# Kernel optimization log

Hardware: AMD Instinct MI355X
Metric: run time of the kernel (lower is better)

Reference implementation:

```python
import jax, jax.numpy as jnp
import numpy as np

D_MODEL = 1024
N_HEADS = 16
D_HEAD = D_MODEL // N_HEADS
B, S = 2, 2048


def setup_inputs() -> dict:
    key = jax.random.key(0)
    ks = jax.random.split(key, 8)
    scale = 1.0 / np.sqrt(D_MODEL)
    return {
        "x": jax.random.normal(ks[0], (B, S, D_MODEL), dtype=jnp.float32),
        "Wq": jax.random.normal(ks[1], (D_MODEL, D_MODEL), dtype=jnp.float32) * scale,
        "bq": jnp.zeros((D_MODEL,), dtype=jnp.float32),
        "Wk": jax.random.normal(ks[2], (D_MODEL, D_MODEL), dtype=jnp.float32) * scale,
        "bk": jnp.zeros((D_MODEL,), dtype=jnp.float32),
        "Wv": jax.random.normal(ks[3], (D_MODEL, D_MODEL), dtype=jnp.float32) * scale,
        "bv": jnp.zeros((D_MODEL,), dtype=jnp.float32),
        "Wo": jax.random.normal(ks[4], (D_MODEL, D_MODEL), dtype=jnp.float32) * scale,
    }


def reference(x, Wq, bq, Wk, bk, Wv, bv, Wo):
    Bsz, Slen, D = x.shape
    # projections -> [B, H, S, Dh]
    def split_heads(t):
        return t.reshape(Bsz, Slen, N_HEADS, D_HEAD).transpose(0, 2, 1, 3)
    q = split_heads(x @ Wq + bq)
    k = split_heads(x @ Wk + bk)
    v = split_heads(x @ Wv + bv)
    scale = jnp.sqrt(jnp.float32(D_HEAD))
    scores = jnp.einsum('bhsd,bhtd->bhst', q, k) / scale  # [B,H,S,S]
    causal_mask = jnp.tril(jnp.ones((Slen, Slen), dtype=jnp.bool_))
    scores = jnp.where(causal_mask, scores, jnp.finfo(scores.dtype).min)
    attn = jax.nn.softmax(scores, axis=-1)
    # deterministic=True path: dropout is identity
    out = jnp.einsum('bhst,bhtd->bhsd', attn, v)
    out = out.transpose(0, 2, 1, 3).reshape(Bsz, Slen, D)
    return out @ Wo
```

## Files before the change

### kernel.cpp

```cpp
#include <hip/hip_runtime.h>
#include <hip/hip_bf16.h>

#define BATCH   2
#define SEQ     2048
#define DMODEL  1024
#define NHEADS  16
#define DHEAD   64
#define MROWS   (BATCH*SEQ)
#define NBH     (BATCH*NHEADS)

typedef float  f32x4  __attribute__((ext_vector_type(4)));
typedef short  s16x4  __attribute__((ext_vector_type(4)));
typedef short  s16x8  __attribute__((ext_vector_type(8)));
typedef __bf16 bf16x8 __attribute__((ext_vector_type(8)));

__device__ __forceinline__ short f2bf(float f) {
  union { float f; unsigned u; } v; v.f = f;
  return (short)((v.u + 0x7fffu + ((v.u >> 16) & 1u)) >> 16);
}
__device__ __forceinline__ float bf2f(short s) {
  union { unsigned u; float f; } v; v.u = ((unsigned)(unsigned short)s) << 16;
  return v.f;
}

__global__ void prep_fused(const float* __restrict__ x, short* __restrict__ xb,
                           const float* __restrict__ Wq, const float* __restrict__ Wk,
                           const float* __restrict__ Wv, const float* __restrict__ Wo,
                           short* __restrict__ WtQKV, short* __restrict__ WtO) {
  __shared__ float t[32][33];
  int z = blockIdx.z;
  int tx = threadIdx.x, ty = threadIdx.y;
  if (z >= 4) {
    int blk = (z - 4) * 1024 + blockIdx.y * 32 + blockIdx.x;
    int i = (blk * 256 + ty * 32 + tx) * 4;
    float4 v = *(const float4*)(x + i);
    s16x4 o = { f2bf(v.x), f2bf(v.y), f2bf(v.z), f2bf(v.w) };
    *(s16x4*)(xb + i) = o;
    return;
  }
  const float* W; short* Wt;
  if      (z == 0) { W = Wq; Wt = WtQKV; }
  else if (z == 1) { W = Wk; Wt = WtQKV + (1u << 20); }
  else if (z == 2) { W = Wv; Wt = WtQKV + (2u << 20); }
  else             { W = Wo; Wt = WtO; }
  int n0 = blockIdx.x * 32, k0 = blockIdx.y * 32;
  #pragma unroll
  for (int i = 0; i < 32; i += 8) t[ty + i][tx] = W[(k0 + ty + i) * DMODEL + n0 + tx];
  __syncthreads();
  #pragma unroll
  for (int i = 0; i < 32; i += 8) Wt[(n0 + ty + i) * DMODEL + k0 + tx] = f2bf(t[tx][ty + i]);
}

template<int MT, int NT, int EPI>
__global__ __launch_bounds__(256) void gemm_bf16(
    const short* __restrict__ A, const short* __restrict__ Bt,
    const float* __restrict__ bq, const float* __restrict__ bk, const float* __restrict__ bv,
    short* __restrict__ qb, short* __restrict__ kb, short* __restrict__ vt,
    float* __restrict__ out)
{
  constexpr int K = DMODEL, BK = 32;
  constexpr int WM = MT / 2, WN = NT / 2;
  constexpr int TM = WM / 16, TN = WN / 16;
  constexpr int CA = MT * BK / 512;
  constexpr int CB = NT * BK / 512;
  constexpr int TP = 136;
  constexpr int SME = (EPI == 0) ? 128 * TP : (MT * BK + NT * BK);
  __shared__ short smem[SME];
  short* la = smem;
  short* lb = smem + MT * BK;
  const int tid = threadIdx.x;
  const int wave = tid >> 6, lane = tid & 63;
  const int quad = lane >> 4, l16 = lane & 15;
  const int wr = wave >> 1, wc = wave & 1;
  const int nx = gridDim.x, ny = gridDim.y;
  const int g = blockIdx.y * nx + blockIdx.x;
  const int xcd = g & 7, rr = g >> 3;
  const int m0 = (xcd * (ny >> 3) + rr / nx) * MT;
  const int n0 = (rr % nx) * NT;
  const int arow = lane >> 2, acol = (lane & 3) * 8;

  f32x4 acc[TM][TN] = {};

  for (int k0 = 0; k0 < K; k0 += BK) {
    for (int c = wave; c < CA; c += 4) {
      const short* gp = A + (m0 + c * 16 + arow) * K + k0 + acol;
      __builtin_amdgcn_global_load_lds((__attribute__((address_space(1))) void*)gp,
                                       (__attribute__((address_space(3))) void*)(la + c * 512),
                                       16, 0, 0);
    }
    for (int c = wave; c < CB; c += 4) {
      const short* gp = Bt + (n0 + c * 16 + arow) * K + k0 + acol;
      __builtin_amdgcn_global_load_lds((__attribute__((address_space(1))) void*)gp,
                                       (__attribute__((address_space(3))) void*)(lb + c * 512),
                                       16, 0, 0);
    }
    __syncthreads();
    bf16x8 af[TM], bfr[TN];
    #pragma unroll
    for (int i = 0; i < TM; ++i)
      af[i] = *(const bf16x8*)&la[(wr * WM + i * 16 + l16) * BK + quad * 8];
    #pragma unroll
    for (int j = 0; j < TN; ++j)
      bfr[j] = *(const bf16x8*)&lb[(wc * WN + j * 16 + l16) * BK + quad * 8];
    #pragma unroll
    for (int i = 0; i < TM; ++i)
      #pragma unroll
      for (int j = 0; j < TN; ++j)
        acc[i][j] = __builtin_amdgcn_mfma_f32_16x16x32_bf16(af[i], bfr[j], acc[i][j], 0, 0, 0);
    __syncthreads();
  }

  if constexpr (EPI == 0) {
    const bool isV = (n0 >= 2 * DMODEL);
    const float* bias; int nbase; float scl;
    if (n0 < DMODEL)          { bias = bq; nbase = 0;          scl = 0.125f * 1.44269504089f; }
    else if (n0 < 2 * DMODEL) { bias = bk; nbase = DMODEL;     scl = 1.f; }
    else                      { bias = bv; nbase = 2 * DMODEL; scl = 1.f; }
    #pragma unroll
    for (int j = 0; j < TN; ++j) {
      int coll = wc * WN + j * 16 + l16;
      float bias_v = bias[n0 - nbase + coll];
      #pragma unroll
      for (int i = 0; i < TM; ++i) {
        int rowl = wr * WM + i * 16 + quad * 4;
        #pragma unroll
        for (int r = 0; r < 4; ++r) {
          short v = f2bf((acc[i][j][r] + bias_v) * scl);
          if (isV) smem[coll * TP + rowl + r] = v;
          else     smem[(rowl + r) * TP + coll] = v;
        }
      }
    }
    __syncthreads();
    const int b = m0 >> 11, s0 = m0 & (SEQ - 1);
    const int rseg = tid & 15, rrow = tid >> 4;
    if (!isV) {
      short* dst = (n0 < DMODEL) ? qb : kb;
      #pragma unroll
      for (int it = 0; it < 8; ++it) {
        int row = it * 16 + rrow;
        int colg = (n0 - nbase) + rseg * 8;
        int h = colg >> 6, d = colg & 63;
        s16x8 v = *(const s16x8*)&smem[row * TP + rseg * 8];
        *(s16x8*)(dst + ((b * NHEADS + h) * SEQ + s0 + row) * DHEAD + d) = v;
      }
    } else {
      #pragma unroll
      for (int it = 0; it < 8; ++it) {
        int drow = it * 16 + rrow;
        int colg = (n0 - nbase) + drow;
        int h = colg >> 6, d = colg & 63;
        s16x8 v = *(const s16x8*)&smem[drow * TP + rseg * 8];
        *(s16x8*)(vt + ((b * NHEADS + h) * DHEAD + d) * SEQ + s0 + rseg * 8) = v;
      }
    }
  } else {
    #pragma unroll
    for (int i = 0; i < TM; ++i)
      #pragma unroll
      for (int r = 0; r < 4; ++r) {
        int mrow = m0 + wr * WM + i * 16 + quad * 4 + r;
        #pragma unroll
        for (int j = 0; j < TN; ++j)
          out[mrow * DMODEL + n0 + wc * WN + j * 16 + l16] = acc[i][j][r];
      }
    (void)bq; (void)bk; (void)bv; (void)qb; (void)kb; (void)vt;
  }
}


__global__ __launch_bounds__(256, 2) void attn_k(
    const short* __restrict__ qbp, const short* __restrict__ kbp,
    const short* __restrict__ vtb, short* __restrict__ oP, float* __restrict__ lP)
{
  __shared__ short kls[2][8192];
  __shared__ short vls[2][8192];
  const int tid = threadIdx.x, wave = tid >> 6, lane = tid & 63;
  const int quad = lane >> 4, l16 = lane & 15;
  const int hi = blockIdx.x >> 8;
  const int q6 = (blockIdx.x >> 6) & 3;
  const int qg = hi ? 7 - q6 : q6;
  const int half = (blockIdx.x >> 5) & 1;
  const int bh = blockIdx.x & 31;
  const int qt1 = qg * 8 + wave * 2;
  const int mF[4] = { qt1 * 16, (qt1 + 1) * 16, (126 - qt1) * 16, (127 - qt1) * 16 };
  const int nch = (127 - 8 * qg) / 4 + 1;
  const short* Q  = qbp + bh * SEQ * DHEAD;
  const short* Kp = kbp + bh * SEQ * DHEAD;
  const short* Vt = vtb + bh * DHEAD * SEQ;

  bf16x8 qf[4][2];
  #pragma unroll
  for (int f = 0; f < 4; ++f) {
    qf[f][0] = *(const bf16x8*)&Q[(mF[f] + l16) * DHEAD + quad * 8];
    qf[f][1] = *(const bf16x8*)&Q[(mF[f] + l16) * DHEAD + 32 + quad * 8];
  }

  float lF[4] = {};
  f32x4 oF[4][4] = {};

  const int vdl = lane >> 3, vsl = lane & 7;

  auto stage1 = [&](int buf, int slot, int t0) {
    #pragma unroll
    for (int j = 0; j < 2; ++j) {
      int g = j * 4 + wave;
      const short* gp = Kp + (t0 + lane) * DHEAD + g * 8;
      __builtin_amdgcn_global_load_lds((__attribute__((address_space(1))) void*)gp,
                                       (__attribute__((address_space(3))) void*)&kls[buf][slot * 4096 + g * 512],
                                       16, 0, 0);
    }
    #pragma unroll
    for (int j = 0; j < 2; ++j) {
      int gd = j * 4 + wave;
      const short* gp = Vt + (gd * 8 + vdl) * SEQ + t0 + ((vsl ^ vdl) * 8);
      __builtin_amdgcn_global_load_lds((__attribute__((address_space(1))) void*)gp,
                                       (__attribute__((address_space(3))) void*)&vls[buf][slot * 4096 + gd * 512],
                                       16, 0, 0);
    }
  };
  auto stagepair = [&](int buf, int cc) {
    stage1(buf, 0, cc * 64);
    if (cc + 2 < nch) stage1(buf, 1, (cc + 2) * 64);
  };

  stagepair(0, half);
  int it = 0;
  for (int cc = half; cc < nch; cc += 4, ++it) {
    __syncthreads();
    if (cc + 4 < nch) stagepair((it + 1) & 1, cc + 4);
    const int buf = it & 1;
    #pragma unroll
    for (int u = 0; u < 2; ++u) {
      const int c = cc + 2 * u;
      if (c < nch) {
        const int t0 = c * 64;
        const int sb = u * 4096;
        #pragma unroll
        for (int t = 0; t < 4; ++t) {
          const int tb = t0 + t * 16;
          if (tb <= mF[3]) {
            bf16x8 kf0 = *(const bf16x8*)&kls[buf][sb + ((0 + quad) * 64 + t * 16 + l16) * 8];
            bf16x8 kf1 = *(const bf16x8*)&kls[buf][sb + ((4 + quad) * 64 + t * 16 + l16) * 8];
            s16x4 vf[4];
            {
              int gsw = ((t * 2 + (quad >> 1)) ^ (l16 & 7));
              #pragma unroll
              for (int dt = 0; dt < 4; ++dt)
                vf[dt] = *(const s16x4*)&vls[buf][sb + ((dt * 16 + l16) * 8 + gsw) * 8 + (quad & 1) * 4];
            }
            #pragma unroll
            for (int f = 0; f < 4; ++f) {
              if (tb <= mF[f]) {
                f32x4 a = {};
                a = __builtin_amdgcn_mfma_f32_16x16x32_bf16(kf0, qf[f][0], a, 0, 0, 0);
                a = __builtin_amdgcn_mfma_f32_16x16x32_bf16(kf1, qf[f][1], a, 0, 0, 0);
                if (tb == mF[f]) {
                  #pragma unroll
                  for (int r = 0; r < 4; ++r)
                    if (quad * 4 + r > l16) a[r] = -1e30f;
                }
                f32x4 p;
                #pragma unroll
                for (int r = 0; r < 4; ++r) p[r] = __builtin_amdgcn_exp2f(a[r]);
                lF[f] += (p[0] + p[1]) + (p[2] + p[3]);
                __hip_bfloat162 c01 = __float22bfloat162_rn(float2{p[0], p[1]});
                __hip_bfloat162 c23 = __float22bfloat162_rn(float2{p[2], p[3]});
                union { unsigned u2[2]; s16x4 s; } pu;
                pu.u2[0] = *(unsigned*)&c01; pu.u2[1] = *(unsigned*)&c23;
                #pragma unroll
                for (int dt = 0; dt < 4; ++dt)
                  oF[f][dt] = __builtin_amdgcn_mfma_f32_16x16x16bf16_1k(pu.s, vf[dt], oF[f][dt], 0, 0, 0);
              }
            }
          }
        }
      }
    }
  }

  float* lD = lP + (half * NBH + bh) * SEQ;
  short* oD = oP + ((half * NBH + bh) * SEQ) * DHEAD;
  #pragma unroll
  for (int f = 0; f < 4; ++f) {
    float l = lF[f];
    l += __shfl_xor(l, 16, 64); l += __shfl_xor(l, 32, 64);
    if (quad == 0) lD[mF[f] + l16] = l;
    #pragma unroll
    for (int r = 0; r < 4; ++r) {
      int s = mF[f] + quad * 4 + r;
      #pragma unroll
      for (int dt = 0; dt < 4; ++dt)
        oD[s * DHEAD + dt * 16 + l16] = f2bf(oF[f][dt][r]);
    }
  }
}

__global__ void attn_merge(const short* __restrict__ oP, const float* __restrict__ lP,
                           short* __restrict__ ob) {
  int idx = blockIdx.x * 256 + threadIdx.x;
  int d8 = idx & 7, s = (idx >> 3) & (SEQ - 1), bh = idx >> 14;
  s16x8 e = *(const s16x8*)&oP[((0   + bh) * SEQ + s) * DHEAD + d8 * 8];
  s16x8 o = *(const s16x8*)&oP[((NBH + bh) * SEQ + s) * DHEAD + d8 * 8];
  float linv = 1.0f / (lP[bh * SEQ + s] + lP[(NBH + bh) * SEQ + s]);
  s16x8 r;
  #pragma unroll
  for (int k = 0; k < 8; ++k) r[k] = f2bf((bf2f(e[k]) + bf2f(o[k])) * linv);
  int b = bh >> 4, h = bh & 15;
  *(s16x8*)&ob[(b * SEQ + s) * DMODEL + h * DHEAD + d8 * 8] = r;
}

extern "C" void kernel_launch(void* const* d_in, const int* in_sizes, int n_in,
                              void* d_out, int out_size, void* d_ws, size_t ws_size,
                              hipStream_t stream) {
  const float* x  = (const float*)d_in[0];
  const float* Wq = (const float*)d_in[1];
  const float* bq = (const float*)d_in[2];
  const float* Wk = (const float*)d_in[3];
  const float* bk = (const float*)d_in[4];
  const float* Wv = (const float*)d_in[5];
  const float* bv = (const float*)d_in[6];
  const float* Wo = (const float*)d_in[7];
  float* out = (float*)d_out;

  char* ws = (char*)d_ws;
  short* xb  = (short*)(ws);
  short* wtq = (short*)(ws + (8u  << 20));
  short* wto = (short*)(ws + (14u << 20));
  short* qb  = (short*)(ws + (16u << 20));
  short* kb  = (short*)(ws + (24u << 20));
  short* vt  = (short*)(ws + (32u << 20));
  short* ob  = (short*)(ws + (40u << 20));
  short* oP  = (short*)(ws + (48u << 20));
  float* lP  = (float*)(ws + (80u << 20));

  prep_fused<<<dim3(32, 32, 8), dim3(32, 8), 0, stream>>>(x, xb, Wq, Wk, Wv, Wo, wtq, wto);

  gemm_bf16<128, 128, 0><<<dim3(3 * DMODEL / 128, MROWS / 128), 256, 0, stream>>>(
      xb, wtq, bq, bk, bv, qb, kb, vt, nullptr);

  attn_k<<<8 * NBH * 2, 256, 0, stream>>>(qb, kb, vt, oP, lP);
  attn_merge<<<NBH * SEQ * 8 / 256, 256, 0, stream>>>(oP, lP, ob);

  gemm_bf16<64, 128, 1><<<dim3(DMODEL / 128, MROWS / 64), 256, 0, stream>>>(
      ob, wto, nullptr, nullptr, nullptr, nullptr, nullptr, nullptr, out);
}
```

Measured before the change: 184.2 us.

## Add dedicated 256x256 double-buffered QKV GEMM kernel with swizzled LDS

Replaces the generic 128x128 QKV projection GEMM with a specialised kernel. The new kernel uses 512 threads, 256x256 tiles and BK=64, with double-buffered direct global-to-LDS loads, an XOR-swizzled LDS layout and prefetch of the next stage that overlaps MFMA work. The epilogue writes out in two halves, applying the bias and head-split/transpose through LDS. The aim is more data reuse per tile and less barrier stall, at the cost of a 128 KB LDS footprint, high register pressure and only 192 blocks for the whole GPU.

```diff
diff --git a/kernel.cpp b/kernel.cpp
--- a/kernel.cpp
+++ b/kernel.cpp
@@ -63,8 +63,7 @@
   constexpr int TM = WM / 16, TN = WN / 16;
   constexpr int CA = MT * BK / 512;
   constexpr int CB = NT * BK / 512;
-  constexpr int TP = 136;
-  constexpr int SME = (EPI == 0) ? 128 * TP : (MT * BK + NT * BK);
+  constexpr int SME = MT * BK + NT * BK;
   __shared__ short smem[SME];
   short* la = smem;
   short* lb = smem + MT * BK;
@@ -110,64 +109,173 @@
     __syncthreads();
   }
 
-  if constexpr (EPI == 0) {
-    const bool isV = (n0 >= 2 * DMODEL);
-    const float* bias; int nbase; float scl;
-    if (n0 < DMODEL)          { bias = bq; nbase = 0;          scl = 0.125f * 1.44269504089f; }
-    else if (n0 < 2 * DMODEL) { bias = bk; nbase = DMODEL;     scl = 1.f; }
-    else                      { bias = bv; nbase = 2 * DMODEL; scl = 1.f; }
-    #pragma unroll
-    for (int j = 0; j < TN; ++j) {
-      int coll = wc * WN + j * 16 + l16;
-      float bias_v = bias[n0 - nbase + coll];
-      #pragma unroll
-      for (int i = 0; i < TM; ++i) {
-        int rowl = wr * WM + i * 16 + quad * 4;
+  #pragma unroll
+  for (int i = 0; i < TM; ++i)
+    #pragma unroll
+    for (int r = 0; r < 4; ++r) {
+      int mrow = m0 + wr * WM + i * 16 + quad * 4 + r;
+      #pragma unroll
+      for (int j = 0; j < TN; ++j)
+        out[mrow * DMODEL + n0 + wc * WN + j * 16 + l16] = acc[i][j][r];
+    }
+  (void)bq; (void)bk; (void)bv; (void)qb; (void)kb; (void)vt;
+}
+
+__global__ __launch_bounds__(512, 2) void gemm_qkv(
+    const short* __restrict__ A, const short* __restrict__ Bt,
+    const float* __restrict__ bq, const float* __restrict__ bk, const float* __restrict__ bv,
+    short* __restrict__ qb, short* __restrict__ kb, short* __restrict__ vt)
+{
+  constexpr int K = DMODEL, BK = 64, NT = K / BK;
+  __shared__ short lds[65536];
+  const int tid = threadIdx.x;
+  const int wave = tid >> 6, lane = tid & 63;
+  const int quad = lane >> 4, l16 = lane & 15;
+  const int wr = wave >> 2, wc = wave & 3;
+
+  const int g  = blockIdx.x;
+  const int s  = (g & 7) * 24 + (g >> 3);
+  const int m0 = (s / 12) * 256, n0 = (s % 12) * 256;
+
+  const int srow = lane >> 3;
+  const int sgl  = (lane & 7) ^ srow;
+  const short* gA = A  + (m0 + wave * 8 + srow) * K + sgl * 8;
+  const short* gB = Bt + (n0 + wave * 8 + srow) * K + sgl * 8;
+
+  auto stage = [&](int buf, int k0) {
+    short* dA = lds + buf * 32768 + wave * 512;
+    short* dB = dA + 16384;
+    #pragma unroll
+    for (int ss = 0; ss < 4; ++ss)
+      __builtin_amdgcn_global_load_lds(
+          (__attribute__((address_space(1))) void*)(gA + ss * 64 * K + k0),
+          (__attribute__((address_space(3))) void*)(dA + ss * 4096), 16, 0, 0);
+    #pragma unroll
+    for (int ss = 0; ss < 4; ++ss)
+      __builtin_amdgcn_global_load_lds(
+          (__attribute__((address_space(1))) void*)(gB + ss * 64 * K + k0),
+          (__attribute__((address_space(3))) void*)(dB + ss * 4096), 16, 0, 0);
+  };
+
+  const int swz = l16 & 7;
+  f32x4 acc[8][4] = {};
+
+  stage(0, 0);
+  stage(1, BK);
+  asm volatile("s_waitcnt vmcnt(0)" ::: "memory");
+  __builtin_amdgcn_sched_barrier(0);
+  __builtin_amdgcn_s_barrier();
+
+  for (int t = 0; t < NT; ++t) {
+    const int cur = t & 1;
+    const short* bA = lds + cur * 32768;
+    const short* bB = bA + 16384;
+
+    bf16x8 a0[4], h0[4], b0[4];
+    #pragma unroll
+    for (int j = 0; j < 4; ++j)
+      b0[j] = *(const bf16x8*)&bB[(wc * 64 + j * 16 + l16) * 64 + (quad ^ swz) * 8];
+    #pragma unroll
+    for (int i = 0; i < 4; ++i) {
+      a0[i] = *(const bf16x8*)&bA[(wr * 128 + i * 16 + l16) * 64 + (quad ^ swz) * 8];
+      h0[i] = *(const bf16x8*)&bA[(wr * 128 + 64 + i * 16 + l16) * 64 + (quad ^ swz) * 8];
+    }
+    __builtin_amdgcn_s_setprio(1);
+    #pragma unroll
+    for (int i = 0; i < 4; ++i)
+      #pragma unroll
+      for (int j = 0; j < 4; ++j) {
+        acc[i][j]     = __builtin_amdgcn_mfma_f32_16x16x32_bf16(a0[i], b0[j], acc[i][j], 0, 0, 0);
+        acc[4 + i][j] = __builtin_amdgcn_mfma_f32_16x16x32_bf16(h0[i], b0[j], acc[4 + i][j], 0, 0, 0);
+      }
+    __builtin_amdgcn_s_setprio(0);
+
+    bf16x8 a1[4], h1[4], b1[4];
+    #pragma unroll
+    for (int j = 0; j < 4; ++j)
+      b1[j] = *(const bf16x8*)&bB[(wc * 64 + j * 16 + l16) * 64 + ((4 | quad) ^ swz) * 8];
+    #pragma unroll
+    for (int i = 0; i < 4; ++i) {
+      a1[i] = *(const bf16x8*)&bA[(wr * 128 + i * 16 + l16) * 64 + ((4 | quad) ^ swz) * 8];
+      h1[i] = *(const bf16x8*)&bA[(wr * 128 + 64 + i * 16 + l16) * 64 + ((4 | quad) ^ swz) * 8];
+    }
+    asm volatile("s_waitcnt lgkmcnt(0)" ::: "memory");
+    __builtin_amdgcn_sched_barrier(0);
+    __builtin_amdgcn_s_barrier();
+    if (t + 2 < NT) stage(cur, (t + 2) * BK);
+
+    __builtin_amdgcn_s_setprio(1);
+    #pragma unroll
+    for (int i = 0; i < 4; ++i)
+      #pragma unroll
+      for (int j = 0; j < 4; ++j) {
+        acc[i][j]     = __builtin_amdgcn_mfma_f32_16x16x32_bf16(a1[i], b1[j], acc[i][j], 0, 0, 0);
+        acc[4 + i][j] = __builtin_amdgcn_mfma_f32_16x16x32_bf16(h1[i], b1[j], acc[4 + i][j], 0, 0, 0);
+      }
+    __builtin_amdgcn_s_setprio(0);
+
+    if (t + 1 < NT) {
+      if (t + 2 < NT) asm volatile("s_waitcnt vmcnt(8)" ::: "memory");
+      else            asm volatile("s_waitcnt vmcnt(0)" ::: "memory");
+      __builtin_amdgcn_sched_barrier(0);
+      __builtin_amdgcn_s_barrier();
+    }
+  }
+
+  const int b = m0 >> 11, s0 = m0 & (SEQ - 1);
+  const int sel = n0 >> 10;
+  const int n0rel = n0 & (DMODEL - 1);
+  const float* bias = (sel == 0) ? bq : (sel == 1) ? bk : bv;
+  const float scl = (sel == 0) ? 0.125f * 1.44269504089f : 1.0f;
+  const bool isV = (sel == 2);
+  short* eT = lds;
+
+  __syncthreads();
+  for (int hp = 0; hp < 2; ++hp) {
+    if ((wc >> 1) == hp) {
+      #pragma unroll
+      for (int j = 0; j < 4; ++j) {
+        int coll = wc * 64 + j * 16 + l16;
+        int cl = coll & 127;
+        float bias_v = bias[n0rel + coll];
         #pragma unroll
-        for (int r = 0; r < 4; ++r) {
-          short v = f2bf((acc[i][j][r] + bias_v) * scl);
-          if (isV) smem[coll * TP + rowl + r] = v;
-          else     smem[(rowl + r) * TP + coll] = v;
+        for (int i = 0; i < 8; ++i) {
+          int rowb = wr * 128 + i * 16 + quad * 4;
+          #pragma unroll
+          for (int r = 0; r < 4; ++r) {
+            short val = f2bf((acc[i][j][r] + bias_v) * scl);
+            if (isV) eT[cl * 264 + rowb + r] = val;
+            else     eT[(rowb + r) * 136 + cl] = val;
+          }
         }
       }
     }
     __syncthreads();
-    const int b = m0 >> 11, s0 = m0 & (SEQ - 1);
-    const int rseg = tid & 15, rrow = tid >> 4;
     if (!isV) {
-      short* dst = (n0 < DMODEL) ? qb : kb;
+      short* dst = (sel == 0) ? qb : kb;
+      const int rseg = tid & 15, rrow = tid >> 4;
       #pragma unroll
       for (int it = 0; it < 8; ++it) {
-        int row = it * 16 + rrow;
-        int colg = (n0 - nbase) + rseg * 8;
+        int row = it * 32 + rrow;
+        int colg = n0rel + hp * 128 + rseg * 8;
         int h = colg >> 6, d = colg & 63;
-        s16x8 v = *(const s16x8*)&smem[row * TP + rseg * 8];
+        s16x8 v = *(const s16x8*)&eT[row * 136 + rseg * 8];
         *(s16x8*)(dst + ((b * NHEADS + h) * SEQ + s0 + row) * DHEAD + d) = v;
       }
     } else {
+      const int sseg = tid & 31, dl0 = tid >> 5;
       #pragma unroll
       for (int it = 0; it < 8; ++it) {
-        int drow = it * 16 + rrow;
-        int colg = (n0 - nbase) + drow;
+        int dloc = it * 16 + dl0;
+        int colg = n0rel + hp * 128 + dloc;
         int h = colg >> 6, d = colg & 63;
-        s16x8 v = *(const s16x8*)&smem[drow * TP + rseg * 8];
-        *(s16x8*)(vt + ((b * NHEADS + h) * DHEAD + d) * SEQ + s0 + rseg * 8) = v;
-      }
-    }
-  } else {
-    #pragma unroll
-    for (int i = 0; i < TM; ++i)
-      #pragma unroll
-      for (int r = 0; r < 4; ++r) {
-        int mrow = m0 + wr * WM + i * 16 + quad * 4 + r;
-        #pragma unroll
-        for (int j = 0; j < TN; ++j)
-          out[mrow * DMODEL + n0 + wc * WN + j * 16 + l16] = acc[i][j][r];
-      }
-    (void)bq; (void)bk; (void)bv; (void)qb; (void)kb; (void)vt;
-  }
-}
-
+        s16x8 v = *(const s16x8*)&eT[dloc * 264 + sseg * 8];
+        *(s16x8*)(vt + ((b * NHEADS + h) * DHEAD + d) * SEQ + s0 + sseg * 8) = v;
+      }
+    }
+    __syncthreads();
+  }
+}
 
 __global__ __launch_bounds__(256, 2) void attn_k(
     const short* __restrict__ qbp, const short* __restrict__ kbp,
@@ -336,8 +444,7 @@
 
   prep_fused<<<dim3(32, 32, 8), dim3(32, 8), 0, stream>>>(x, xb, Wq, Wk, Wv, Wo, wtq, wto);
 
-  gemm_bf16<128, 128, 0><<<dim3(3 * DMODEL / 128, MROWS / 128), 256, 0, stream>>>(
-      xb, wtq, bq, bk, bv, qb, kb, vt, nullptr);
+  gemm_qkv<<<dim3(192), 512, 0, stream>>>(xb, wtq, bq, bk, bv, qb, kb, vt);
 
   attn_k<<<8 * NBH * 2, 256, 0, stream>>>(qb, kb, vt, oP, lP);
   attn_merge<<<NBH * SEQ * 8 / 256, 256, 0, stream>>>(oP, lP, ob);
```

New measurement: 189.1 us. +2.7%, slower.
